# Performance work log

Hardware: AMD Instinct MI355X
Metric: run time of the kernel (lower is better)

The kernel has to match this reference:

```python
import jax, jax.numpy as jnp
import numpy as np

N_IN = 2048
N_OUT = 2048
RANK = 64
NUM_ITER = 4  # Newton-Schulz iterations, matches default num_iter=4


def setup_inputs() -> dict:
    key = jax.random.key(0)
    k1, k2, k3 = jax.random.split(key, 3)
    # scale U,V modestly so A = UV^T - VU^T is well-conditioned (mimics orthogonal init scale)
    scale = 1.0 / np.sqrt(N_IN)
    return {
        "input": jax.random.normal(k1, (8, 2048, N_IN), dtype=jnp.float32),
        "U": jax.random.normal(k2, (N_IN, RANK), dtype=jnp.float32) * scale,
        "V": jax.random.normal(k3, (N_IN, RANK), dtype=jnp.float32) * scale,
    }


def _orthogonal_weight(U, V):
    # A = U V^T - V U^T  (skew-symmetric, rank <= 2*rank)
    A = U @ V.T - V @ U.T              # [n, n]
    I = jnp.eye(N_IN, dtype=A.dtype)
    B = I - A
    X = I
    for _ in range(NUM_ITER):          # Newton-Schulz iteration for B^{-1}
        X = X @ (2.0 * I - B @ X)
    W_square = (I + A) @ X             # Cayley transform (I+A)(I-A)^{-1} approx
    return W_square[:N_OUT, :N_IN]


def reference(input, U, V):
    W = _orthogonal_weight(U, V)       # [out, in]
    # F.linear(input, W) = input @ W.T
    return jnp.einsum("bsi,oi->bso", input, W)
```

## Files before the change

### kernel.cpp

```cpp
#include <hip/hip_runtime.h>
#include <hip/hip_bf16.h>
#include <cstdint>
#include <cstddef>

#define NIN   2048
#define RANK  64
#define R2    128
#define NROWS 16384

typedef __bf16 bf16x8 __attribute__((ext_vector_type(8)));
typedef float  f32x4  __attribute__((ext_vector_type(4)));
typedef unsigned short u16x8 __attribute__((ext_vector_type(8)));

__device__ __forceinline__ unsigned short f2bf(float f) {
  union { float f; unsigned u; } x; x.f = f;
  return (unsigned short)((x.u + 0x7fffu + ((x.u >> 16) & 1u)) >> 16);
}

__device__ __forceinline__ void smallGemm(const float* __restrict__ A,
                                          const float* __restrict__ B,
                                          float* __restrict__ O,
                                          float a, float b, int t, int tid) {
  int i = (t >> 3) * 16 + (tid >> 4);
  int j = (t & 7) * 16 + (tid & 15);
  float acc = 0.f;
#pragma unroll 8
  for (int k = 0; k < R2; ++k) {
    float av = A[i * R2 + k]; if (k == i) av += a;
    float bv = B[k * R2 + j]; if (k == j) bv += b;
    acc += av * bv;
  }
  O[i * R2 + j] = acc;
}

__global__ __launch_bounds__(512) void k_prep(const float* __restrict__ U,
                                              const float* __restrict__ V,
                                              unsigned short* __restrict__ Mf,
                                              unsigned short* __restrict__ Mrf,
                                              float* __restrict__ G) {
  __shared__ float red[512];
  int b = blockIdx.x, tid = threadIdx.x;
  if (b < 64) {
    int CI = b * 512 + tid;
    int lane = CI & 63, J = (CI >> 6) & 63, t = CI >> 12;
    int n = t * 16 + (lane & 15);
    int k0 = J * 32 + (lane >> 4) * 8;
    const float* src = (n < RANK) ? (U + n) : (V + (n - RANK));
    u16x8 h;
#pragma unroll
    for (int e = 0; e < 8; ++e) h[e] = f2bf(src[(size_t)(k0 + e) * RANK]);
    *(u16x8*)(Mf + (size_t)CI * 8) = h;
  } else if (b < 128) {
    int tile = b - 64;
    int bi = tile >> 3, bj = tile & 7;
    int sub = tid >> 8, t256 = tid & 255;
    int ty = t256 >> 4, tx = t256 & 15;
    int i = bi * 16 + ty, j = bj * 16 + tx;
    const float* Ai = (i < RANK) ? (U + i) : (V + (i - RANK));
    const float* Aj = (j < RANK) ? (U + j) : (V + (j - RANK));
    int k0 = sub * 1024;
    float p0 = 0.f, p1 = 0.f, p2 = 0.f, p3 = 0.f;
#pragma unroll 4
    for (int k = k0; k < k0 + 1024; k += 4) {
      p0 += Ai[(size_t)k * RANK]       * Aj[(size_t)k * RANK];
      p1 += Ai[(size_t)(k + 1) * RANK] * Aj[(size_t)(k + 1) * RANK];
      p2 += Ai[(size_t)(k + 2) * RANK] * Aj[(size_t)(k + 2) * RANK];
      p3 += Ai[(size_t)(k + 3) * RANK] * Aj[(size_t)(k + 3) * RANK];
    }
    red[tid] = (p0 + p1) + (p2 + p3);
    __syncthreads();
    if (sub == 0) {
      float s = red[t256] + red[256 + t256];
      if (i < RANK) G[(i + RANK) * R2 + j] = -s;
      else          G[(i - RANK) * R2 + j] =  s;
    }
  } else {
    int CI = (b - 128) * 512 + tid;
    int lane = CI & 63, rest = CI >> 6;
    int lr = lane & 15, lg = lane >> 4;
    int J = rest & 3, t_ = rest >> 2;
    int i = t_ * 16 + lr, j0 = J * 32 + lg * 8;
    const float* src = (j0 < RANK) ? (U + (size_t)i * RANK + j0)
                                   : (V + (size_t)i * RANK + (j0 - RANK));
    float4 f0 = *(const float4*)src, f1 = *(const float4*)(src + 4);
    u16x8 h;
    h[0] = f2bf(f0.x); h[1] = f2bf(f0.y); h[2] = f2bf(f0.z); h[3] = f2bf(f0.w);
    h[4] = f2bf(f1.x); h[5] = f2bf(f1.y); h[6] = f2bf(f1.z); h[7] = f2bf(f1.w);
    *(u16x8*)(Mrf + (size_t)CI * 8) = h;
  }
}

struct SOp { const float* A; const float* B; float* O; float a, b; };
struct SOps { SOp op[3]; };
__global__ void k_small(SOps ops) {
  SOp o = ops.op[blockIdx.x >> 6];
  smallGemm(o.A, o.B, o.O, o.a, o.b, blockIdx.x & 63, threadIdx.x);
}

__global__ __launch_bounds__(256, 3) void k_T1(const float* __restrict__ input,
                                               const unsigned short* __restrict__ Mf,
                                               unsigned short* __restrict__ T1bf,
                                               const float* __restrict__ G,
                                               float* __restrict__ G2) {
  __shared__ __align__(16) unsigned char lds[33792];
  if (blockIdx.x >= 1024) {
    smallGemm(G, G, G2, 0.f, 0.f, blockIdx.x - 1024, threadIdx.x);
    return;
  }
  const int tid = threadIdx.x, lane = tid & 63, w = tid >> 6;
  const int lr = lane & 15, lg = lane >> 4;
  const int row0 = blockIdx.x * 16;
  unsigned char* ab0 = lds + w * 8192;

  f32x4 acc[8] = {};
  const float* gbase = input + (size_t)row0 * NIN + w * 512;
  const int Jbase = w * 16;
  float4 s0[4], s1[4];
  bf16x8 bx[8], by[8];

#define T1_SLOAD(KT)                                                          \
  _Pragma("unroll") for (int c = 0; c < 4; ++c) {                             \
    int id = c * 64 + lane; int r = id >> 4, C = id & 15;                     \
    const float* g = gbase + (size_t)r * NIN + (KT) * 128 + C * 8;            \
    s0[c] = *(const float4*)g; s1[c] = *(const float4*)(g + 4);               \
  }
#define T1_SWRITE(BUF)                                                        \
  _Pragma("unroll") for (int c = 0; c < 4; ++c) {                             \
    int id = c * 64 + lane; int r = id >> 4, C = id & 15;                     \
    u16x8 h;                                                                  \
    h[0] = f2bf(s0[c].x); h[1] = f2bf(s0[c].y);                               \
    h[2] = f2bf(s0[c].z); h[3] = f2bf(s0[c].w);                               \
    h[4] = f2bf(s1[c].x); h[5] = f2bf(s1[c].y);                               \
    h[6] = f2bf(s1[c].z); h[7] = f2bf(s1[c].w);                               \
    *(u16x8*)(ab0 + (BUF) * 4096 + r * 256 + ((C ^ (r & 7)) << 4)) = h;       \
  }
#define T1_BLOAD(P, S)                                                        \
  _Pragma("unroll") for (int t = 0; t < 8; ++t)                               \
    P[t] = *(const bf16x8*)(Mf + ((size_t)(t * 64 + Jbase + (S)) * 64 + lane) * 8);

  T1_SLOAD(0);
  T1_SWRITE(0);
  T1_BLOAD(bx, 0);
#pragma unroll
  for (int s = 0; s < 16; ++s) {
    const int kt = s >> 2, sub = s & 3, buf = kt & 1;
    if (sub == 0 && kt < 3) { T1_SLOAD(kt + 1); }
    bf16x8 a = *(const bf16x8*)(ab0 + buf * 4096 + lr * 256 + (((sub * 4 + lg) ^ (lr & 7)) << 4));
    if (s < 15) { if (s & 1) { T1_BLOAD(bx, s + 1); } else { T1_BLOAD(by, s + 1); } }
#pragma unroll
    for (int t = 0; t < 8; ++t) {
      bf16x8 bcur = (s & 1) ? by[t] : bx[t];
      acc[t] = __builtin_amdgcn_mfma_f32_16x16x32_bf16(a, bcur, acc[t], 0, 0, 0);
    }
    if (sub == 2 && kt < 3) { T1_SWRITE(buf ^ 1); }
  }

  __syncthreads();
  float* rbw = (float*)lds + (size_t)w * 2112;
#pragma unroll
  for (int t = 0; t < 8; ++t) {
    int col = t * 16 + lr;
#pragma unroll
    for (int e = 0; e < 4; ++e) rbw[(lg * 4 + e) * 132 + col] = acc[t][e];
  }
  __syncthreads();
  {
    int r = tid >> 4, c8 = tid & 15;
    f32x4 a0 = {}, a1 = {};
#pragma unroll
    for (int ww = 0; ww < 4; ++ww) {
      const float* p = (const float*)lds + (size_t)ww * 2112 + r * 132 + c8 * 8;
      a0 += *(const f32x4*)p;
      a1 += *(const f32x4*)(p + 4);
    }
    u16x8 o;
#pragma unroll
    for (int i = 0; i < 4; ++i) { o[i] = f2bf(a0[i]); o[4 + i] = f2bf(a1[i]); }
    *(u16x8*)(T1bf + (size_t)(row0 + r) * R2 + c8 * 8) = o;
  }
}

__global__ __launch_bounds__(256, 3) void k_OUT(const float* __restrict__ input,
                                                const unsigned short* __restrict__ T1bf,
                                                const float* __restrict__ Hm,
                                                const float* __restrict__ G15m,
                                                const unsigned short* __restrict__ Mrf,
                                                float* __restrict__ out) {
  __shared__ __align__(16) unsigned char lds[43008];
  unsigned char* cbuf = lds;
  unsigned char* t2buf = lds + 34816;
  const int tid = threadIdx.x, lane = tid & 63, w = tid >> 6;
  const int lr = lane & 15, lg = lane >> 4;
  const int row0 = blockIdx.x * 32;

#pragma unroll
  for (int it = 0; it < 8; ++it) {
    int id = it * 256 + tid;
    int k = id >> 4, j8 = id & 15, j0 = j8 * 8;
    int jj0 = (j0 < RANK) ? j0 + RANK : j0 - RANK;
    float sgn = (j0 < RANK) ? -1.f : 1.f;
    const float* hp = Hm + k * R2 + jj0;
    const float* gp = G15m + k * R2 + jj0;
    float4 h0 = *(const float4*)hp, h1 = *(const float4*)(hp + 4);
    float4 g0 = *(const float4*)gp, g1 = *(const float4*)(gp + 4);
    u16x8 cv;
    cv[0] = f2bf(sgn * (2.f * h0.x - g0.x));
    cv[1] = f2bf(sgn * (2.f * h0.y - g0.y));
    cv[2] = f2bf(sgn * (2.f * h0.z - g0.z));
    cv[3] = f2bf(sgn * (2.f * h0.w - g0.w));
    cv[4] = f2bf(sgn * (2.f * h1.x - g1.x));
    cv[5] = f2bf(sgn * (2.f * h1.y - g1.y));
    cv[6] = f2bf(sgn * (2.f * h1.z - g1.z));
    cv[7] = f2bf(sgn * (2.f * h1.w - g1.w));
    *(u16x8*)(cbuf + k * 256 + ((j8 ^ (k & 7)) << 4)) = cv;
  }
  bf16x8 t1f[2][4];
#pragma unroll
  for (int R = 0; R < 2; ++R)
#pragma unroll
    for (int J = 0; J < 4; ++J)
      t1f[R][J] = *(const bf16x8*)(T1bf + (size_t)(row0 + R * 16 + lr) * R2 + J * 32 + lg * 8);
  __syncthreads();

#pragma unroll
  for (int kk = 0; kk < 2; ++kk) {
    int kct = w * 2 + kk;
    int kc = kct * 16 + lr;
    f32x4 a2[2] = {};
#pragma unroll
    for (int jkt = 0; jkt < 4; ++jkt) {
      bf16x8 cf = *(const bf16x8*)(cbuf + kc * 256 + (((jkt * 4 + lg) ^ (kc & 7)) << 4));
#pragma unroll
      for (int R = 0; R < 2; ++R)
        a2[R] = __builtin_amdgcn_mfma_f32_16x16x32_bf16(cf, t1f[R][jkt], a2[R], 0, 0, 0);
    }
#pragma unroll
    for (int R = 0; R < 2; ++R) {
      int r = R * 16 + lr;
      ushort4 p;
      p.x = f2bf(a2[R][0]); p.y = f2bf(a2[R][1]);
      p.z = f2bf(a2[R][2]); p.w = f2bf(a2[R][3]);
      int gran = kct * 2 + (lg >> 1), off = (lg & 1) * 8;
      *(ushort4*)(t2buf + r * 256 + ((gran ^ (r & 7)) << 4) + off) = p;
    }
  }
  __syncthreads();

  bf16x8 bq[2][4];
#pragma unroll
  for (int R = 0; R < 2; ++R)
#pragma unroll
    for (int J = 0; J < 4; ++J) {
      int row = R * 16 + lr;
      bq[R][J] = *(const bf16x8*)(t2buf + row * 256 + (((J * 4 + lg) ^ (row & 7)) << 4));
    }

  float* obufw = (float*)(lds + w * 8704);
  bf16x8 xd[4], yd[4];
#define O_DLOAD(P, TTI)                                                       \
  _Pragma("unroll") for (int J = 0; J < 4; ++J)                               \
    P[J] = *(const bf16x8*)(Mrf + ((size_t)((w * 32 + (TTI)) * 4 + J) * 64 + lane) * 8);

  O_DLOAD(xd, 0);
#pragma unroll
  for (int g = 0; g < 8; ++g) {
#pragma unroll
    for (int tt = 0; tt < 4; ++tt) {
      const int tti = g * 4 + tt;
      if (tti < 31) { if (tti & 1) { O_DLOAD(xd, tti + 1); } else { O_DLOAD(yd, tti + 1); } }
#pragma unroll
      for (int R = 0; R < 2; ++R) {
        f32x4 o = {};
#pragma unroll
        for (int J = 0; J < 4; ++J) {
          bf16x8 d = (tti & 1) ? yd[J] : xd[J];
          o = __builtin_amdgcn_mfma_f32_16x16x32_bf16(d, bq[R][J], o, 0, 0, 0);
        }
        *(f32x4*)&obufw[(R * 16 + lr) * 68 + tt * 16 + lg * 4] = o;
      }
    }
#pragma unroll
    for (int c = 0; c < 8; ++c) {
      int id = c * 64 + lane, r = id >> 4, cc = id & 15;
      f32x4 v = *(const f32x4*)&obufw[r * 68 + cc * 4];
      int grow = row0 + r, gcol = w * 512 + g * 64 + cc * 4;
      float4 inv = *(const float4*)(input + (size_t)grow * NIN + gcol);
      float4 res = { v[0] + inv.x, v[1] + inv.y, v[2] + inv.z, v[3] + inv.w };
      *(float4*)(out + (size_t)grow * NIN + gcol) = res;
    }
  }
}

extern "C" void kernel_launch(void* const* d_in, const int* in_sizes, int n_in,
                              void* d_out, int out_size, void* d_ws, size_t ws_size,
                              hipStream_t stream) {
  const float* input = (const float*)d_in[0];
  const float* U     = (const float*)d_in[1];
  const float* V     = (const float*)d_in[2];
  float* out = (float*)d_out;
  char* ws = (char*)d_ws;

  float* mats = (float*)ws;
  float* G   = mats + 0 * 16384;
  float* G2  = mats + 1 * 16384;
  float* G3  = mats + 2 * 16384;
  float* G4  = mats + 3 * 16384;
  float* G7  = mats + 4 * 16384;
  float* G8  = mats + 5 * 16384;
  float* H12 = mats + 6 * 16384;
  float* H124= mats + 7 * 16384;
  float* H   = mats + 8 * 16384;
  float* G15 = mats + 9 * 16384;
  unsigned short* Mf   = (unsigned short*)(ws + 10 * 65536);
  unsigned short* Mrf  = (unsigned short*)(ws + 10 * 65536 + 524288);
  unsigned short* T1bf = (unsigned short*)(ws + 10 * 65536 + 2 * 524288);

  k_prep<<<192, 512, 0, stream>>>(U, V, Mf, Mrf, G);
  k_T1<<<1088, 256, 0, stream>>>(input, Mf, T1bf, G, G2);

  { SOps o = {{ {G2, G2, G4, 0.f, 0.f}, {G2, G, G3, 0.f, 0.f}, {G, G2, H12, 1.f, 1.f} }};
    k_small<<<192, 256, 0, stream>>>(o); }
  { SOps o = {{ {G4, G4, G8, 0.f, 0.f}, {G3, G4, G7, 0.f, 0.f}, {H12, G4, H124, 0.f, 1.f} }};
    k_small<<<192, 256, 0, stream>>>(o); }
  { SOps o = {{ {G7, G8, G15, 0.f, 0.f}, {H124, G8, H, 0.f, 1.f}, {nullptr,nullptr,nullptr,0.f,0.f} }};
    k_small<<<128, 256, 0, stream>>>(o); }

  k_OUT<<<512, 256, 0, stream>>>(input, T1bf, H, G15, Mrf, out);
}
```

Measured before the change: 140.1 us.

## Fuse small-matrix Newton-Schulz chain into T1 kernel with atomic counter dependencies

Moves the three separate small 128x128 GEMM launches into the front of the k_T1 grid as 512 extra blocks. Each stage waits on a global atomic counter set by the previous stage, while the T1 GEMM blocks run alongside. This removes three kernel launches and their gaps and overlaps the latency-bound chain with the bandwidth-heavy T1 work. It relies on low-index blocks being scheduled first, so spinning blocks can occupy CUs, and it adds a counter reset in k_prep.

```diff
diff --git a/kernel.cpp b/kernel.cpp
--- a/kernel.cpp
+++ b/kernel.cpp
@@ -33,13 +33,31 @@
   O[i * R2 + j] = acc;
 }
 
+__device__ __forceinline__ void signalCnt(int* c) {
+  __syncthreads();
+  if (threadIdx.x == 0) {
+    __threadfence();
+    __hip_atomic_fetch_add(c, 1, __ATOMIC_RELEASE, __HIP_MEMORY_SCOPE_AGENT);
+  }
+}
+__device__ __forceinline__ void waitCnt(int* c, int target) {
+  if (threadIdx.x == 0) {
+    while (__hip_atomic_load(c, __ATOMIC_RELAXED, __HIP_MEMORY_SCOPE_AGENT) < target)
+      __builtin_amdgcn_s_sleep(16);
+    (void)__hip_atomic_load(c, __ATOMIC_ACQUIRE, __HIP_MEMORY_SCOPE_AGENT);
+  }
+  __syncthreads();
+}
+
 __global__ __launch_bounds__(512) void k_prep(const float* __restrict__ U,
                                               const float* __restrict__ V,
                                               unsigned short* __restrict__ Mf,
                                               unsigned short* __restrict__ Mrf,
-                                              float* __restrict__ G) {
+                                              float* __restrict__ G,
+                                              int* __restrict__ cnt) {
   __shared__ float red[512];
   int b = blockIdx.x, tid = threadIdx.x;
+  if (b == 0 && tid < 4) cnt[tid] = 0;
   if (b < 64) {
     int CI = b * 512 + tid;
     int lane = CI & 63, J = (CI >> 6) & 63, t = CI >> 12;
@@ -90,26 +108,52 @@
   }
 }
 
-struct SOp { const float* A; const float* B; float* O; float a, b; };
-struct SOps { SOp op[3]; };
-__global__ void k_small(SOps ops) {
-  SOp o = ops.op[blockIdx.x >> 6];
-  smallGemm(o.A, o.B, o.O, o.a, o.b, blockIdx.x & 63, threadIdx.x);
-}
-
 __global__ __launch_bounds__(256, 3) void k_T1(const float* __restrict__ input,
                                                const unsigned short* __restrict__ Mf,
                                                unsigned short* __restrict__ T1bf,
-                                               const float* __restrict__ G,
-                                               float* __restrict__ G2) {
+                                               float* __restrict__ mats,
+                                               int* __restrict__ cnt) {
   __shared__ __align__(16) unsigned char lds[33792];
-  if (blockIdx.x >= 1024) {
-    smallGemm(G, G, G2, 0.f, 0.f, blockIdx.x - 1024, threadIdx.x);
+  if (blockIdx.x < 576) {
+    const int cb = blockIdx.x, tid = threadIdx.x;
+    float* G_   = mats;
+    float* G2_  = mats + 1 * 16384;
+    float* G3_  = mats + 2 * 16384;
+    float* G4_  = mats + 3 * 16384;
+    float* G7_  = mats + 4 * 16384;
+    float* G8_  = mats + 5 * 16384;
+    float* H12_ = mats + 6 * 16384;
+    float* H124_= mats + 7 * 16384;
+    float* H_   = mats + 8 * 16384;
+    float* G15_ = mats + 9 * 16384;
+    if (cb < 64) {
+      smallGemm(G_, G_, G2_, 0.f, 0.f, cb, tid);
+      signalCnt(&cnt[0]);
+    } else if (cb < 256) {
+      int t = (cb - 64) & 63, op = (cb - 64) >> 6;
+      waitCnt(&cnt[0], 64);
+      if (op == 0)      smallGemm(G2_, G2_, G4_,  0.f, 0.f, t, tid);
+      else if (op == 1) smallGemm(G2_, G_,  G3_,  0.f, 0.f, t, tid);
+      else              smallGemm(G_,  G2_, H12_, 1.f, 1.f, t, tid);
+      signalCnt(&cnt[1]);
+    } else if (cb < 448) {
+      int t = (cb - 256) & 63, op = (cb - 256) >> 6;
+      waitCnt(&cnt[1], 192);
+      if (op == 0)      smallGemm(G4_,  G4_, G8_,   0.f, 0.f, t, tid);
+      else if (op == 1) smallGemm(G3_,  G4_, G7_,   0.f, 0.f, t, tid);
+      else              smallGemm(H12_, G4_, H124_, 0.f, 1.f, t, tid);
+      signalCnt(&cnt[2]);
+    } else {
+      int t = (cb - 448) & 63, op = (cb - 448) >> 6;
+      waitCnt(&cnt[2], 192);
+      if (op == 0) smallGemm(G7_,   G8_, G15_, 0.f, 0.f, t, tid);
+      else         smallGemm(H124_, G8_, H_,   0.f, 1.f, t, tid);
+    }
     return;
   }
   const int tid = threadIdx.x, lane = tid & 63, w = tid >> 6;
   const int lr = lane & 15, lg = lane >> 4;
-  const int row0 = blockIdx.x * 16;
+  const int row0 = (blockIdx.x - 576) * 16;
   unsigned char* ab0 = lds + w * 8192;
 
   f32x4 acc[8] = {};
@@ -302,28 +346,14 @@
 
   float* mats = (float*)ws;
   float* G   = mats + 0 * 16384;
-  float* G2  = mats + 1 * 16384;
-  float* G3  = mats + 2 * 16384;
-  float* G4  = mats + 3 * 16384;
-  float* G7  = mats + 4 * 16384;
-  float* G8  = mats + 5 * 16384;
-  float* H12 = mats + 6 * 16384;
-  float* H124= mats + 7 * 16384;
   float* H   = mats + 8 * 16384;
   float* G15 = mats + 9 * 16384;
   unsigned short* Mf   = (unsigned short*)(ws + 10 * 65536);
   unsigned short* Mrf  = (unsigned short*)(ws + 10 * 65536 + 524288);
   unsigned short* T1bf = (unsigned short*)(ws + 10 * 65536 + 2 * 524288);
-
-  k_prep<<<192, 512, 0, stream>>>(U, V, Mf, Mrf, G);
-  k_T1<<<1088, 256, 0, stream>>>(input, Mf, T1bf, G, G2);
-
-  { SOps o = {{ {G2, G2, G4, 0.f, 0.f}, {G2, G, G3, 0.f, 0.f}, {G, G2, H12, 1.f, 1.f} }};
-    k_small<<<192, 256, 0, stream>>>(o); }
-  { SOps o = {{ {G4, G4, G8, 0.f, 0.f}, {G3, G4, G7, 0.f, 0.f}, {H12, G4, H124, 0.f, 1.f} }};
-    k_small<<<192, 256, 0, stream>>>(o); }
-  { SOps o = {{ {G7, G8, G15, 0.f, 0.f}, {H124, G8, H, 0.f, 1.f}, {nullptr,nullptr,nullptr,0.f,0.f} }};
-    k_small<<<128, 256, 0, stream>>>(o); }
-
+  int* cnt = (int*)(ws + 10 * 65536 + 2 * 524288 + 4194304);
+
+  k_prep<<<192, 512, 0, stream>>>(U, V, Mf, Mrf, G, cnt);
+  k_T1<<<1600, 256, 0, stream>>>(input, Mf, T1bf, mats, cnt);
   k_OUT<<<512, 256, 0, stream>>>(input, T1bf, H, G15, Mrf, out);
 }
```

Result: slower. 190.0 us (+35.6%).

## Fold final small 128x128 GEMM stage into output kernel via MFMA

Applied to the files above, without the earlier changes.

Removes the third k_small launch that computed G15 and H from G7, G8 and H124. Each k_OUT block now recomputes the coefficient matrix itself with bf16 MFMAs, using a bf16 fragment-layout copy of G8 written by the preceding k_small. This saves one kernel launch and a dependent stage, but every one of the 512 output blocks redoes a small GEMM, and the product is now formed in bf16 rather than fp32, which may reduce accuracy.

```diff
diff --git a/kernel.cpp b/kernel.cpp
--- a/kernel.cpp
+++ b/kernel.cpp
@@ -20,6 +20,7 @@
 __device__ __forceinline__ void smallGemm(const float* __restrict__ A,
                                           const float* __restrict__ B,
                                           float* __restrict__ O,
+                                          unsigned short* __restrict__ Obf,
                                           float a, float b, int t, int tid) {
   int i = (t >> 3) * 16 + (tid >> 4);
   int j = (t & 7) * 16 + (tid & 15);
@@ -31,6 +32,10 @@
     acc += av * bv;
   }
   O[i * R2 + j] = acc;
+  if (Obf) {
+    int t_ = j >> 4, lr = j & 15, J = i >> 5, lg = (i >> 3) & 3, e = i & 7;
+    Obf[((size_t)(t_ * 4 + J) * 64 + lg * 16 + lr) * 8 + e] = f2bf(acc);
+  }
 }
 
 __global__ __launch_bounds__(512) void k_prep(const float* __restrict__ U,
@@ -90,11 +95,11 @@
   }
 }
 
-struct SOp { const float* A; const float* B; float* O; float a, b; };
+struct SOp { const float* A; const float* B; float* O; unsigned short* Obf; float a, b; };
 struct SOps { SOp op[3]; };
 __global__ void k_small(SOps ops) {
   SOp o = ops.op[blockIdx.x >> 6];
-  smallGemm(o.A, o.B, o.O, o.a, o.b, blockIdx.x & 63, threadIdx.x);
+  smallGemm(o.A, o.B, o.O, o.Obf, o.a, o.b, blockIdx.x & 63, threadIdx.x);
 }
 
 __global__ __launch_bounds__(256, 3) void k_T1(const float* __restrict__ input,
@@ -104,7 +109,7 @@
                                                float* __restrict__ G2) {
   __shared__ __align__(16) unsigned char lds[33792];
   if (blockIdx.x >= 1024) {
-    smallGemm(G, G, G2, 0.f, 0.f, blockIdx.x - 1024, threadIdx.x);
+    smallGemm(G, G, G2, nullptr, 0.f, 0.f, blockIdx.x - 1024, threadIdx.x);
     return;
   }
   const int tid = threadIdx.x, lane = tid & 63, w = tid >> 6;
@@ -182,8 +187,9 @@
 
 __global__ __launch_bounds__(256, 3) void k_OUT(const float* __restrict__ input,
                                                 const unsigned short* __restrict__ T1bf,
-                                                const float* __restrict__ Hm,
-                                                const float* __restrict__ G15m,
+                                                const float* __restrict__ H124,
+                                                const float* __restrict__ G7,
+                                                const unsigned short* __restrict__ g8tf,
                                                 const unsigned short* __restrict__ Mrf,
                                                 float* __restrict__ out) {
   __shared__ __align__(16) unsigned char lds[43008];
@@ -193,33 +199,53 @@
   const int lr = lane & 15, lg = lane >> 4;
   const int row0 = blockIdx.x * 32;
 
-#pragma unroll
-  for (int it = 0; it < 8; ++it) {
-    int id = it * 256 + tid;
-    int k = id >> 4, j8 = id & 15, j0 = j8 * 8;
-    int jj0 = (j0 < RANK) ? j0 + RANK : j0 - RANK;
-    float sgn = (j0 < RANK) ? -1.f : 1.f;
-    const float* hp = Hm + k * R2 + jj0;
-    const float* gp = G15m + k * R2 + jj0;
-    float4 h0 = *(const float4*)hp, h1 = *(const float4*)(hp + 4);
-    float4 g0 = *(const float4*)gp, g1 = *(const float4*)(gp + 4);
-    u16x8 cv;
-    cv[0] = f2bf(sgn * (2.f * h0.x - g0.x));
-    cv[1] = f2bf(sgn * (2.f * h0.y - g0.y));
-    cv[2] = f2bf(sgn * (2.f * h0.z - g0.z));
-    cv[3] = f2bf(sgn * (2.f * h0.w - g0.w));
-    cv[4] = f2bf(sgn * (2.f * h1.x - g1.x));
-    cv[5] = f2bf(sgn * (2.f * h1.y - g1.y));
-    cv[6] = f2bf(sgn * (2.f * h1.z - g1.z));
-    cv[7] = f2bf(sgn * (2.f * h1.w - g1.w));
-    *(u16x8*)(cbuf + k * 256 + ((j8 ^ (k & 7)) << 4)) = cv;
-  }
   bf16x8 t1f[2][4];
 #pragma unroll
   for (int R = 0; R < 2; ++R)
 #pragma unroll
     for (int J = 0; J < 4; ++J)
       t1f[R][J] = *(const bf16x8*)(T1bf + (size_t)(row0 + R * 16 + lr) * R2 + J * 32 + lg * 8);
+
+#pragma unroll
+  for (int kk = 0; kk < 2; ++kk) {
+    int kct = w * 2 + kk;
+    int krow = kct * 16 + lr;
+    bf16x8 qf[4];
+#pragma unroll
+    for (int ms = 0; ms < 4; ++ms) {
+      int m0 = ms * 32 + lg * 8;
+      const float* hp = H124 + (size_t)krow * R2 + m0;
+      const float* gp = G7   + (size_t)krow * R2 + m0;
+      float4 h0 = *(const float4*)hp, h1 = *(const float4*)(hp + 4);
+      float4 g0 = *(const float4*)gp, g1 = *(const float4*)(gp + 4);
+      u16x8 qv;
+      qv[0] = f2bf(2.f * h0.x - g0.x); qv[1] = f2bf(2.f * h0.y - g0.y);
+      qv[2] = f2bf(2.f * h0.z - g0.z); qv[3] = f2bf(2.f * h0.w - g0.w);
+      qv[4] = f2bf(2.f * h1.x - g1.x); qv[5] = f2bf(2.f * h1.y - g1.y);
+      qv[6] = f2bf(2.f * h1.z - g1.z); qv[7] = f2bf(2.f * h1.w - g1.w);
+      qf[ms] = __builtin_bit_cast(bf16x8, qv);
+    }
+#pragma unroll
+    for (int jt = 0; jt < 8; ++jt) {
+      f32x4 a = {};
+#pragma unroll
+      for (int ms = 0; ms < 4; ++ms) {
+        bf16x8 gfr = *(const bf16x8*)(g8tf + ((size_t)(jt * 4 + ms) * 64 + lane) * 8);
+        a = __builtin_amdgcn_mfma_f32_16x16x32_bf16(gfr, qf[ms], a, 0, 0, 0);
+      }
+      int j0 = jt * 16 + lg * 4;
+      float4 h = *(const float4*)(H124 + (size_t)krow * R2 + j0);
+      float sgn = (j0 >= RANK) ? -1.f : 1.f;
+      ushort4 p;
+      p.x = f2bf(sgn * (a[0] + 2.f * h.x));
+      p.y = f2bf(sgn * (a[1] + 2.f * h.y));
+      p.z = f2bf(sgn * (a[2] + 2.f * h.z));
+      p.w = f2bf(sgn * (a[3] + 2.f * h.w));
+      int gran = (jt * 2 + (lg >> 1)) ^ 8;
+      int off = (lg & 1) * 8;
+      *(ushort4*)(cbuf + krow * 256 + ((gran ^ (krow & 7)) << 4) + off) = p;
+    }
+  }
   __syncthreads();
 
 #pragma unroll
@@ -309,21 +335,18 @@
   float* G8  = mats + 5 * 16384;
   float* H12 = mats + 6 * 16384;
   float* H124= mats + 7 * 16384;
-  float* H   = mats + 8 * 16384;
-  float* G15 = mats + 9 * 16384;
   unsigned short* Mf   = (unsigned short*)(ws + 10 * 65536);
   unsigned short* Mrf  = (unsigned short*)(ws + 10 * 65536 + 524288);
   unsigned short* T1bf = (unsigned short*)(ws + 10 * 65536 + 2 * 524288);
+  unsigned short* G8tf = (unsigned short*)(ws + 10 * 65536 + 2 * 524288 + 4194304);
 
   k_prep<<<192, 512, 0, stream>>>(U, V, Mf, Mrf, G);
   k_T1<<<1088, 256, 0, stream>>>(input, Mf, T1bf, G, G2);
 
-  { SOps o = {{ {G2, G2, G4, 0.f, 0.f}, {G2, G, G3, 0.f, 0.f}, {G, G2, H12, 1.f, 1.f} }};
+  { SOps o = {{ {G2, G2, G4, nullptr, 0.f, 0.f}, {G2, G, G3, nullptr, 0.f, 0.f}, {G, G2, H12, nullptr, 1.f, 1.f} }};
     k_small<<<192, 256, 0, stream>>>(o); }
-  { SOps o = {{ {G4, G4, G8, 0.f, 0.f}, {G3, G4, G7, 0.f, 0.f}, {H12, G4, H124, 0.f, 1.f} }};
+  { SOps o = {{ {G4, G4, G8, G8tf, 0.f, 0.f}, {G3, G4, G7, nullptr, 0.f, 0.f}, {H12, G4, H124, nullptr, 0.f, 1.f} }};
     k_small<<<192, 256, 0, stream>>>(o); }
-  { SOps o = {{ {G7, G8, G15, 0.f, 0.f}, {H124, G8, H, 0.f, 1.f}, {nullptr,nullptr,nullptr,0.f,0.f} }};
-    k_small<<<128, 256, 0, stream>>>(o); }
-
-  k_OUT<<<512, 256, 0, stream>>>(input, T1bf, H, G15, Mrf, out);
-}
+
+  k_OUT<<<512, 256, 0, stream>>>(input, T1bf, H124, G7, G8tf, Mrf, out);
+}
```

Measured after the change: 149.1 us. +6.5%, slower.
